# Kernel tuning notes

Hardware: AMD Instinct MI355X
Metric: run time of the kernel (lower is better)

## Reference

```python
import jax, jax.numpy as jnp
import numpy as np

R, S, H, L = 4096, 64, 256, 3  # rays, samples/ray, mlp width, n hidden-to-hidden layers
FAR_DELTA = 1e10


def setup_inputs() -> dict:
    key = jax.random.key(0)
    ks = jax.random.split(key, 16)
    points = jax.random.normal(ks[0], (R, S, 3), dtype=jnp.float32)
    dirs = jax.random.normal(ks[1], (R, S, 3), dtype=jnp.float32)
    dirs = dirs / jnp.linalg.norm(dirs, axis=-1, keepdims=True)
    # sorted depths in a [2, 6] near/far range (monotone along sample axis)
    z_vals = jnp.sort(2.0 + 4.0 * jax.random.uniform(ks[2], (R, S), dtype=jnp.float32), axis=-1)
    time = jax.random.uniform(ks[3], (R, S), dtype=jnp.float32)

    def w(k, shape):
        return 0.05 * jax.random.normal(k, shape, dtype=jnp.float32)

    return {
        'points': points, 'dirs': dirs, 'z_vals': z_vals, 'time': time,
        'sW_in': w(ks[4], (6, H)),  'sb_in': jnp.zeros((H,), jnp.float32),
        'sW_h':  w(ks[5], (L, H, H)), 'sb_h': jnp.zeros((L, H), jnp.float32),
        'sW_out': w(ks[6], (H, 4)), 'sb_out': jnp.zeros((4,), jnp.float32),
        'dW_in': w(ks[7], (7, H)),  'db_in': jnp.zeros((H,), jnp.float32),
        'dW_h':  w(ks[8], (L, H, H)), 'db_h': jnp.zeros((L, H), jnp.float32),
        'dW_out': w(ks[9], (H, 5)), 'db_out': jnp.zeros((5,), jnp.float32),
    }


def _mlp(x, W_in, b_in, W_h, b_h, W_out, b_out):
    h = jax.nn.relu(x @ W_in + b_in)
    for i in range(W_h.shape[0]):  # fixed small layer count
        h = jax.nn.relu(h @ W_h[i] + b_h[i])
    return h @ W_out + b_out


def _compute_weights(sigma, z_vals):
    delta = z_vals[..., 1:] - z_vals[..., :-1]
    delta = jnp.concatenate([delta, jnp.full_like(delta[..., :1], FAR_DELTA)], axis=-1)
    alpha = 1.0 - jnp.exp(-sigma * delta)
    trans = jnp.cumprod(
        jnp.concatenate([jnp.ones_like(alpha[..., :1]), 1.0 - alpha + 1e-10], axis=-1),
        axis=-1)[..., :-1]
    return alpha * trans


def reference(points, dirs, z_vals, time,
              sW_in, sb_in, sW_h, sb_h, sW_out, sb_out,
              dW_in, db_in, dW_h, db_h, dW_out, db_out):
    static_out = _mlp(jnp.concatenate([points, dirs], axis=-1),
                      sW_in, sb_in, sW_h, sb_h, sW_out, sb_out)          # [R,S,4]
    dynamic_out = _mlp(jnp.concatenate([points, dirs, time[..., None]], axis=-1),
                       dW_in, db_in, dW_h, db_h, dW_out, db_out)         # [R,S,5]

    static_sigma = static_out[..., 0]
    static_rgb = jax.nn.sigmoid(static_out[..., 1:4])
    dynamic_sigma = dynamic_out[..., 0]
    dynamic_rgb = jax.nn.sigmoid(dynamic_out[..., 1:4])
    bw = jax.nn.sigmoid(dynamic_out[..., 4])                             # [R,S]

    sigma = (1.0 - bw) * static_sigma + bw * dynamic_sigma               # [R,S]
    rgb = (1.0 - bw)[..., None] * static_rgb + bw[..., None] * dynamic_rgb  # [R,S,3]

    weights = _compute_weights(sigma, z_vals)                            # [R,S]
    rgb_map = jnp.sum(weights[..., None] * rgb, axis=-2)                 # [R,3]
    depth_map = jnp.sum(weights * z_vals, axis=-1)                       # [R]
    return (rgb_map, depth_map, weights, (1.0 - bw) * weights, bw * weights)
```

## Files before the change

### kernel.cpp

```cpp
#include <hip/hip_runtime.h>

#define R_ 4096
#define S_ 64
#define H_ 256
#define N_ (R_ * S_)
#define FARD 1e10f

typedef __attribute__((ext_vector_type(4))) float f32x4;
typedef __attribute__((ext_vector_type(8))) short short8;
typedef __attribute__((ext_vector_type(8))) int i32x8;

union U8 { short8 s; uint4 u; };
union V8 { i32x8 v; uint4 q[2]; long long d[4]; };

__device__ __forceinline__ unsigned int cvt_pk_bf16(float lo, float hi) {
    unsigned int r;
    asm("v_cvt_pk_bf16_f32 %0, %1, %2" : "=v"(r) : "v"(lo), "v"(hi));
    return r;
}
__device__ __forceinline__ unsigned short f2bf(float f) {
    unsigned int x = __float_as_uint(f);
    x += 0x7fffu + ((x >> 16) & 1u);
    return (unsigned short)(x >> 16);
}
__device__ __forceinline__ unsigned int pk4_fp8(float a0, float a1, float a2, float a3) {
    unsigned int lo, hi;
    asm("v_cvt_pk_fp8_f32 %0, %1, %2" : "=v"(lo) : "v"(a0), "v"(a1));
    asm("v_cvt_pk_fp8_f32 %0, %1, %2" : "=v"(hi) : "v"(a2), "v"(a3));
    return (lo & 0xffffu) | (hi << 16);
}
__device__ __forceinline__ unsigned char f2fp8(float v) {
    unsigned int r;
    asm("v_cvt_pk_fp8_f32 %0, %1, %2" : "=v"(r) : "v"(v), "v"(0.0f));
    return (unsigned char)(r & 0xff);
}
__device__ __forceinline__ float sigmoidf_(float x) { return 1.0f / (1.0f + expf(-x)); }

__device__ __forceinline__ int sw_byte(int row, int col) {
    return (row << 8) + (col ^ ((row & 15) << 3));
}

typedef const __attribute__((address_space(1))) unsigned char* gas1;
typedef __attribute__((address_space(3))) unsigned char* las3;
__device__ __forceinline__ void stage64k(const unsigned char* g, unsigned char* l, int tid) {
#pragma unroll
    for (int i = 0; i < 8; ++i)
        __builtin_amdgcn_global_load_lds((gas1)(g + i * 8192 + tid * 16),
                                         (las3)(l + i * 8192 + tid * 16), 16, 0, 0);
}

__device__ void hidden_layer(unsigned char* act, unsigned char* wbuf,
                             const unsigned char* __restrict__ next_panel,
                             const float* __restrict__ bias, int lane, int wv, int tid)
{
    const int m0 = lane & 15;
    const int q  = lane >> 4;
    const int nw = wv << 5;

    f32x4 acc[2][4];
#pragma unroll
    for (int nt = 0; nt < 2; ++nt) {
        const float4 bv = *(const float4*)&bias[nw + nt * 16 + 4 * q];
#pragma unroll
        for (int mt = 0; mt < 4; ++mt) {
            acc[nt][mt][0] = bv.x; acc[nt][mt][1] = bv.y;
            acc[nt][mt][2] = bv.z; acc[nt][mt][3] = bv.w;
        }
    }

    __builtin_amdgcn_s_setprio(1);
#pragma unroll
    for (int s = 0; s < 2; ++s) {
        V8 A[2];
#pragma unroll
        for (int nt = 0; nt < 2; ++nt) {
            const int t = wv * 4 + nt * 2 + s;
            A[nt].q[0] = *(const uint4*)(wbuf + t * 2048 + lane * 16);
            A[nt].q[1] = *(const uint4*)(wbuf + t * 2048 + 1024 + lane * 16);
        }
#pragma unroll
        for (int mt = 0; mt < 4; ++mt) {
            V8 B;
#pragma unroll
            for (int j = 0; j < 4; ++j)
                B.d[j] = *(const long long*)(act + sw_byte(mt * 16 + m0,
                                                           s * 128 + q * 32 + 8 * j));
#pragma unroll
            for (int nt = 0; nt < 2; ++nt)
                acc[nt][mt] = __builtin_amdgcn_mfma_scale_f32_16x16x128_f8f6f4(
                    A[nt].v, B.v, acc[nt][mt], 0, 0,
                    0, 0x7F7F7F7Fu, 0, 0x7F7F7F7Fu);
        }
    }
    __builtin_amdgcn_s_setprio(0);
    __syncthreads();
    if (next_panel) stage64k(next_panel, wbuf, tid);
#pragma unroll
    for (int nt = 0; nt < 2; ++nt)
#pragma unroll
        for (int mt = 0; mt < 4; ++mt) {
            f32x4 a = acc[nt][mt];
            unsigned int u = pk4_fp8(fmaxf(a[0], 0.f), fmaxf(a[1], 0.f),
                                     fmaxf(a[2], 0.f), fmaxf(a[3], 0.f));
            *(unsigned int*)(act + sw_byte(mt * 16 + m0, nw + nt * 16 + 4 * q)) = u;
        }
    __syncthreads();
}

__device__ void input_compute(const float* __restrict__ pts, const float* __restrict__ drs,
                              const float* __restrict__ tv,
                              const short* __restrict__ WinT, const float* __restrict__ bin,
                              unsigned int pk[8], int base, int lane, int wv)
{
    const int m0 = lane & 15;
    const int q  = lane >> 4;
    const int nw = wv << 5;

    short8 B[4];
#pragma unroll
    for (int mt = 0; mt < 4; ++mt) {
        U8 ub;
        if (q == 0) {
            const int s = base + mt * 16 + m0;
            float p0 = pts[s * 3 + 0], p1 = pts[s * 3 + 1], p2 = pts[s * 3 + 2];
            float e0 = drs[s * 3 + 0], e1 = drs[s * 3 + 1], e2 = drs[s * 3 + 2];
            float t  = tv[s];
            ub.u = make_uint4(cvt_pk_bf16(p0, p1), cvt_pk_bf16(p2, e0),
                              cvt_pk_bf16(e1, e2), cvt_pk_bf16(t, 0.f));
        } else {
            ub.u = make_uint4(0, 0, 0, 0);
        }
        B[mt] = ub.s;
    }

    f32x4 acc[2][4];
#pragma unroll
    for (int nt = 0; nt < 2; ++nt) {
        const float4 bv = *(const float4*)&bin[nw + nt * 16 + 4 * q];
#pragma unroll
        for (int mt = 0; mt < 4; ++mt) {
            acc[nt][mt][0] = bv.x; acc[nt][mt][1] = bv.y;
            acc[nt][mt][2] = bv.z; acc[nt][mt][3] = bv.w;
        }
    }
#pragma unroll
    for (int nt = 0; nt < 2; ++nt) {
        short8 A = *(const short8*)&WinT[(nw + nt * 16 + m0) * 32 + 8 * q];
#pragma unroll
        for (int mt = 0; mt < 4; ++mt)
            acc[nt][mt] = __builtin_amdgcn_mfma_f32_16x16x32_bf16(A, B[mt], acc[nt][mt], 0, 0, 0);
    }
#pragma unroll
    for (int nt = 0; nt < 2; ++nt)
#pragma unroll
        for (int mt = 0; mt < 4; ++mt) {
            f32x4 a = acc[nt][mt];
            pk[nt * 4 + mt] = pk4_fp8(fmaxf(a[0], 0.f), fmaxf(a[1], 0.f),
                                      fmaxf(a[2], 0.f), fmaxf(a[3], 0.f));
        }
}

__device__ __forceinline__ void input_store(unsigned char* act, const unsigned int pk[8],
                                            int lane, int wv)
{
    const int m0 = lane & 15;
    const int q  = lane >> 4;
    const int nw = wv << 5;
#pragma unroll
    for (int nt = 0; nt < 2; ++nt)
#pragma unroll
        for (int mt = 0; mt < 4; ++mt)
            *(unsigned int*)(act + sw_byte(mt * 16 + m0, nw + nt * 16 + 4 * q)) = pk[nt * 4 + mt];
}

template <int OUTD>
__device__ void out_mfma(const unsigned char* act, const unsigned char* __restrict__ WoT,
                         const float* __restrict__ bout, float* o, int lane, int wv)
{
    const int m0 = lane & 15;
    const int q  = lane >> 4;
    const int m  = (wv << 4) + m0;

    f32x4 acc = {0.f, 0.f, 0.f, 0.f};
#pragma unroll
    for (int ks = 0; ks < 8; ++ks) {
        long long A = *(const long long*)(WoT + m0 * H_ + ks * 32 + 8 * q);
        long long B = *(const long long*)(act + sw_byte(m, ks * 32 + 8 * q));
        acc = __builtin_amdgcn_mfma_f32_16x16x32_fp8_fp8(A, B, acc, 0, 0, 0);
    }
    if (q == 0) {
        o[0] = acc[0] + bout[0]; o[1] = acc[1] + bout[1];
        o[2] = acc[2] + bout[2]; o[3] = acc[3] + bout[3];
    }
    if (OUTD == 5 && q == 1) o[4] = acc[0] + bout[4];
}

__global__ __launch_bounds__(512, 4) void nerf_kernel(
    const float* __restrict__ points, const float* __restrict__ dirs,
    const float* __restrict__ z_vals, const float* __restrict__ timev,
    const float* __restrict__ sbin, const float* __restrict__ sbh, const float* __restrict__ sbout,
    const float* __restrict__ dbin, const float* __restrict__ dbh, const float* __restrict__ dbout,
    const unsigned char* __restrict__ wsb,
    float* __restrict__ out)
{
    __shared__ __align__(16) unsigned char wbuf[65536];
    __shared__ __align__(16) unsigned char act[64 * H_];

    const int tid  = threadIdx.x;
    const int lane = tid & 63;
    const int wv   = tid >> 6;
    const int ray  = blockIdx.x;
    const int base = ray * 64;

    const unsigned char* sW8   = wsb;
    const unsigned char* dW8   = wsb + 196608;
    const short* sWinT = (const short*)(wsb + 393216);
    const short* dWinT = (const short*)(wsb + 409600);
    const unsigned char* sWoT8 = wsb + 425984;
    const unsigned char* dWoT8 = wsb + 430080;

    stage64k(sW8 + 0 * 65536, wbuf, tid);
    {
        unsigned int pk[8];
        input_compute(points, dirs, timev, sWinT, sbin, pk, base, lane, wv);
        input_store(act, pk, lane, wv);
    }
    __syncthreads();

    hidden_layer(act, wbuf, sW8 + 1 * 65536, sbh + 0 * H_, lane, wv, tid);
    hidden_layer(act, wbuf, sW8 + 2 * 65536, sbh + 1 * H_, lane, wv, tid);
    hidden_layer(act, wbuf, dW8 + 0 * 65536, sbh + 2 * H_, lane, wv, tid);

    float so[4];
    unsigned int dpk[8];
    input_compute(points, dirs, timev, dWinT, dbin, dpk, base, lane, wv);
    if (wv < 4) out_mfma<4>(act, sWoT8, sbout, so, lane, wv);
    __syncthreads();
    input_store(act, dpk, lane, wv);
    __syncthreads();

    hidden_layer(act, wbuf, dW8 + 1 * 65536, dbh + 0 * H_, lane, wv, tid);
    hidden_layer(act, wbuf, dW8 + 2 * 65536, dbh + 1 * H_, lane, wv, tid);
    hidden_layer(act, wbuf, nullptr,         dbh + 2 * H_, lane, wv, tid);

    float dox[5];
    if (wv < 4) out_mfma<5>(act, dWoT8, dbout, dox, lane, wv);
    __syncthreads();

    float* mixb = (float*)act;
    if (wv < 4) {
        const int m0 = lane & 15;
        const int q  = lane >> 4;
        const int m  = (wv << 4) + m0;
        if (q == 0) {
            mixb[m * 9 + 0] = so[0];  mixb[m * 9 + 1] = so[1];
            mixb[m * 9 + 2] = so[2];  mixb[m * 9 + 3] = so[3];
            mixb[m * 9 + 4] = dox[0]; mixb[m * 9 + 5] = dox[1];
            mixb[m * 9 + 6] = dox[2]; mixb[m * 9 + 7] = dox[3];
        }
        if (q == 1) mixb[m * 9 + 8] = dox[4];
    }
    __syncthreads();

    if (tid < 64) {
        const int s = tid;
        float so0 = mixb[s * 9 + 0], so1 = mixb[s * 9 + 1];
        float so2 = mixb[s * 9 + 2], so3 = mixb[s * 9 + 3];
        float d0 = mixb[s * 9 + 4], d1 = mixb[s * 9 + 5], d2 = mixb[s * 9 + 6];
        float d3 = mixb[s * 9 + 7], d4 = mixb[s * 9 + 8];

        float bw  = sigmoidf_(d4);
        float omb = 1.f - bw;
        float sigma = omb * so0 + bw * d0;
        float cr = omb * sigmoidf_(so1) + bw * sigmoidf_(d1);
        float cg = omb * sigmoidf_(so2) + bw * sigmoidf_(d2);
        float cb = omb * sigmoidf_(so3) + bw * sigmoidf_(d3);

        float z  = z_vals[base + s];
        float zn = __shfl_down(z, 1);
        float delta = (s < 63) ? (zn - z) : FARD;
        float ex    = fminf(-sigma * delta, 60.0f);
        float alpha = 1.f - expf(ex);
        float f     = 1.f - alpha + 1e-10f;
        float p = f;
#pragma unroll
        for (int d = 1; d < 64; d <<= 1) {
            float pu = __shfl_up(p, d);
            if (s >= d) p *= pu;
        }
        float T = (s == 0) ? 1.f : __shfl_up(p, 1);
        float w = alpha * T;

        float* rgb_map   = out;
        float* depth_map = out + R_ * 3;
        float* weights   = out + R_ * 4;
        float* swei      = weights + N_;
        float* dwei      = swei + N_;
        weights[base + s] = w;
        swei[base + s]    = omb * w;
        dwei[base + s]    = bw * w;

        float c0 = w * cr, c1 = w * cg, c2 = w * cb, dd = w * z;
#pragma unroll
        for (int d = 32; d >= 1; d >>= 1) {
            c0 += __shfl_down(c0, d);
            c1 += __shfl_down(c1, d);
            c2 += __shfl_down(c2, d);
            dd += __shfl_down(dd, d);
        }
        if (s == 0) {
            rgb_map[ray * 3 + 0] = c0;
            rgb_map[ray * 3 + 1] = c1;
            rgb_map[ray * 3 + 2] = c2;
            depth_map[ray] = dd;
        }
    }
}

__global__ void convert_weights(const float* __restrict__ sWh, const float* __restrict__ dWh,
                                const float* __restrict__ sWin, const float* __restrict__ dWin,
                                const float* __restrict__ sWout, const float* __restrict__ dWout,
                                unsigned char* __restrict__ ws)
{
    int idx = blockIdx.x * 256 + threadIdx.x;
    if (idx < 393216) {
        int which = idx >= 196608;
        int rem   = which ? idx - 196608 : idx;
        int l = rem >> 16, e = rem & 65535;
        int t = e >> 11, r2 = e & 2047;
        int h = r2 >> 10, r3 = r2 & 1023;
        int ln = r3 >> 4, b = r3 & 15;
        int wv = t >> 2, nt = (t >> 1) & 1, s = t & 1;
        int n = wv * 32 + nt * 16 + (ln & 15);
        int k = s * 128 + (ln >> 4) * 32 + h * 16 + b;
        const float* W = which ? dWh : sWh;
        ws[idx] = f2fp8(W[l * 65536 + k * 256 + n]);
    } else if (idx < 409600) {
        int j = idx - 393216;
        int which = j >= 8192;
        int e = j & 8191;
        int n = e >> 5, k = e & 31;
        int ink = which ? 7 : 6;
        const float* W = which ? dWin : sWin;
        float v = (k < ink) ? W[k * 256 + n] : 0.f;
        ((short*)(ws + 393216))[j] = (short)f2bf(v);
    } else {
        int j = idx - 409600;
        int which = j >= 4096;
        int e = j & 4095;
        int o = e >> 8, k = e & 255;
        int outd = which ? 5 : 4;
        const float* W = which ? dWout : sWout;
        float v = (o < outd) ? W[k * outd + o] : 0.f;
        ws[425984 + j] = f2fp8(v);
    }
}

extern "C" void kernel_launch(void* const* d_in, const int* in_sizes, int n_in,
                              void* d_out, int out_size, void* d_ws, size_t ws_size,
                              hipStream_t stream)
{
    const float* points = (const float*)d_in[0];
    const float* dirs   = (const float*)d_in[1];
    const float* z_vals = (const float*)d_in[2];
    const float* timev  = (const float*)d_in[3];
    const float* sWin   = (const float*)d_in[4];
    const float* sbin   = (const float*)d_in[5];
    const float* sWh    = (const float*)d_in[6];
    const float* sbh    = (const float*)d_in[7];
    const float* sWout  = (const float*)d_in[8];
    const float* sbout  = (const float*)d_in[9];
    const float* dWin   = (const float*)d_in[10];
    const float* dbin   = (const float*)d_in[11];
    const float* dWh    = (const float*)d_in[12];
    const float* dbh    = (const float*)d_in[13];
    const float* dWout  = (const float*)d_in[14];
    const float* dbout  = (const float*)d_in[15];

    unsigned char* wsb = (unsigned char*)d_ws;

    convert_weights<<<1632, 256, 0, stream>>>(sWh, dWh, sWin, dWin, sWout, dWout, wsb);

    nerf_kernel<<<R_, 512, 0, stream>>>(
        points, dirs, z_vals, timev,
        sbin, sbh, sbout, dbin, dbh, dbout,
        wsb, (float*)d_out);
}
```

Before: 188.6 us.

## Store activations in MFMA fragment-native LDS layout for 128-bit loads

Activations in LDS are now written in the per-lane fragment order that the 16x16x128 fp8 MFMA consumes, replacing the XOR-swizzled row-major layout. Each B operand is then read with two 16-byte loads instead of four 8-byte loads. The output projection also moves from eight 16x16x32 fp8 MFMAs to two 16x16x128 scaled MFMAs, with the output weights repacked into the matching layout. The intended gain is fewer LDS instructions and fewer MFMA issues per layer, at the cost of possible bank conflicts on the scattered 4-byte fragment stores.

```diff
diff --git a/kernel.cpp b/kernel.cpp
--- a/kernel.cpp
+++ b/kernel.cpp
@@ -11,7 +11,7 @@
 typedef __attribute__((ext_vector_type(8))) int i32x8;
 
 union U8 { short8 s; uint4 u; };
-union V8 { i32x8 v; uint4 q[2]; long long d[4]; };
+union V8 { i32x8 v; uint4 q[2]; };
 
 __device__ __forceinline__ unsigned int cvt_pk_bf16(float lo, float hi) {
     unsigned int r;
@@ -36,10 +36,6 @@
 }
 __device__ __forceinline__ float sigmoidf_(float x) { return 1.0f / (1.0f + expf(-x)); }
 
-__device__ __forceinline__ int sw_byte(int row, int col) {
-    return (row << 8) + (col ^ ((row & 15) << 3));
-}
-
 typedef const __attribute__((address_space(1))) unsigned char* gas1;
 typedef __attribute__((address_space(3))) unsigned char* las3;
 __device__ __forceinline__ void stage64k(const unsigned char* g, unsigned char* l, int tid) {
@@ -47,6 +43,22 @@
     for (int i = 0; i < 8; ++i)
         __builtin_amdgcn_global_load_lds((gas1)(g + i * 8192 + tid * 16),
                                          (las3)(l + i * 8192 + tid * 16), 16, 0, 0);
+}
+
+
+__device__ __forceinline__ void store_act_frag(unsigned char* act, const unsigned int pk[8],
+                                               int lane, int wv)
+{
+    const int m0 = lane & 15;
+    const int q  = lane >> 4;
+    const int sp = wv >> 2;
+    const int c4 = (wv & 3) << 4;
+#pragma unroll
+    for (int nt = 0; nt < 2; ++nt)
+#pragma unroll
+        for (int mt = 0; mt < 4; ++mt)
+            *(unsigned int*)(act + (mt * 2 + sp) * 2048 + nt * 1024 +
+                             (c4 + m0) * 16 + 4 * q) = pk[nt * 4 + mt];
 }
 
 __device__ void hidden_layer(unsigned char* act, unsigned char* wbuf,
@@ -81,10 +93,8 @@
 #pragma unroll
         for (int mt = 0; mt < 4; ++mt) {
             V8 B;
-#pragma unroll
-            for (int j = 0; j < 4; ++j)
-                B.d[j] = *(const long long*)(act + sw_byte(mt * 16 + m0,
-                                                           s * 128 + q * 32 + 8 * j));
+            B.q[0] = *(const uint4*)(act + (mt * 2 + s) * 2048 + lane * 16);
+            B.q[1] = *(const uint4*)(act + (mt * 2 + s) * 2048 + 1024 + lane * 16);
 #pragma unroll
             for (int nt = 0; nt < 2; ++nt)
                 acc[nt][mt] = __builtin_amdgcn_mfma_scale_f32_16x16x128_f8f6f4(
@@ -95,15 +105,16 @@
     __builtin_amdgcn_s_setprio(0);
     __syncthreads();
     if (next_panel) stage64k(next_panel, wbuf, tid);
+    unsigned int pk[8];
 #pragma unroll
     for (int nt = 0; nt < 2; ++nt)
 #pragma unroll
         for (int mt = 0; mt < 4; ++mt) {
             f32x4 a = acc[nt][mt];
-            unsigned int u = pk4_fp8(fmaxf(a[0], 0.f), fmaxf(a[1], 0.f),
-                                     fmaxf(a[2], 0.f), fmaxf(a[3], 0.f));
-            *(unsigned int*)(act + sw_byte(mt * 16 + m0, nw + nt * 16 + 4 * q)) = u;
-        }
+            pk[nt * 4 + mt] = pk4_fp8(fmaxf(a[0], 0.f), fmaxf(a[1], 0.f),
+                                      fmaxf(a[2], 0.f), fmaxf(a[3], 0.f));
+        }
+    store_act_frag(act, pk, lane, wv);
     __syncthreads();
 }
 
@@ -160,33 +171,22 @@
         }
 }
 
-__device__ __forceinline__ void input_store(unsigned char* act, const unsigned int pk[8],
-                                            int lane, int wv)
-{
-    const int m0 = lane & 15;
-    const int q  = lane >> 4;
-    const int nw = wv << 5;
-#pragma unroll
-    for (int nt = 0; nt < 2; ++nt)
-#pragma unroll
-        for (int mt = 0; mt < 4; ++mt)
-            *(unsigned int*)(act + sw_byte(mt * 16 + m0, nw + nt * 16 + 4 * q)) = pk[nt * 4 + mt];
-}
-
 template <int OUTD>
 __device__ void out_mfma(const unsigned char* act, const unsigned char* __restrict__ WoT,
                          const float* __restrict__ bout, float* o, int lane, int wv)
 {
-    const int m0 = lane & 15;
-    const int q  = lane >> 4;
-    const int m  = (wv << 4) + m0;
+    const int q = lane >> 4;
 
     f32x4 acc = {0.f, 0.f, 0.f, 0.f};
 #pragma unroll
-    for (int ks = 0; ks < 8; ++ks) {
-        long long A = *(const long long*)(WoT + m0 * H_ + ks * 32 + 8 * q);
-        long long B = *(const long long*)(act + sw_byte(m, ks * 32 + 8 * q));
-        acc = __builtin_amdgcn_mfma_f32_16x16x32_fp8_fp8(A, B, acc, 0, 0, 0);
+    for (int s = 0; s < 2; ++s) {
+        V8 A, B;
+        A.q[0] = *(const uint4*)(WoT + s * 2048 + lane * 16);
+        A.q[1] = *(const uint4*)(WoT + s * 2048 + 1024 + lane * 16);
+        B.q[0] = *(const uint4*)(act + (wv * 2 + s) * 2048 + lane * 16);
+        B.q[1] = *(const uint4*)(act + (wv * 2 + s) * 2048 + 1024 + lane * 16);
+        acc = __builtin_amdgcn_mfma_scale_f32_16x16x128_f8f6f4(
+            A.v, B.v, acc, 0, 0, 0, 0x7F7F7F7Fu, 0, 0x7F7F7F7Fu);
     }
     if (q == 0) {
         o[0] = acc[0] + bout[0]; o[1] = acc[1] + bout[1];
@@ -223,7 +223,7 @@
     {
         unsigned int pk[8];
         input_compute(points, dirs, timev, sWinT, sbin, pk, base, lane, wv);
-        input_store(act, pk, lane, wv);
+        store_act_frag(act, pk, lane, wv);
     }
     __syncthreads();
 
@@ -236,7 +236,7 @@
     input_compute(points, dirs, timev, dWinT, dbin, dpk, base, lane, wv);
     if (wv < 4) out_mfma<4>(act, sWoT8, sbout, so, lane, wv);
     __syncthreads();
-    input_store(act, dpk, lane, wv);
+    store_act_frag(act, dpk, lane, wv);
     __syncthreads();
 
     hidden_layer(act, wbuf, dW8 + 1 * 65536, dbh + 0 * H_, lane, wv, tid);
@@ -348,11 +348,15 @@
         int j = idx - 409600;
         int which = j >= 4096;
         int e = j & 4095;
-        int o = e >> 8, k = e & 255;
+        int s = e >> 11, r2 = e & 2047;
+        int h = r2 >> 10, r3 = r2 & 1023;
+        int ln = r3 >> 4, b = r3 & 15;
+        int o = ln & 15;
+        int k = s * 128 + (ln >> 4) * 32 + h * 16 + b;
         int outd = which ? 5 : 4;
         const float* W = which ? dWout : sWout;
         float v = (o < outd) ? W[k * outd + o] : 0.f;
-        ws[425984 + j] = f2fp8(v);
+        ws[425984 + (which ? 4096 : 0) + e] = f2fp8(v);
     }
 }
 
```

Result: faster. 158.8 us (median of 2 runs) (-15.8%).
